# Optimization experiments

Measured on AMD Instinct MI355X. Metric: run time of the kernel, lower is better.

The kernel has to match this reference:

```python
import jax, jax.numpy as jnp
import numpy as np


def setup_inputs() -> dict:
    key = jax.random.key(0)
    k1, k2, k3, k4, k5 = jax.random.split(key, 5)
    N, E, C_in, C_out = 100000, 1600000, 64, 64
    x = jax.random.normal(k1, (N, C_in), dtype=jnp.float32)
    edge_index = jax.random.randint(k2, (2, E), 0, N, dtype=jnp.int64)
    edge_weight = jax.random.uniform(k3, (E,), dtype=jnp.float32)
    # Xavier-uniform Linear weights [out, in], zero biases (matches reset_parameters)
    bound = float(np.sqrt(6.0 / (C_in + C_out)))
    W_self = jax.random.uniform(k4, (C_out, C_in), dtype=jnp.float32, minval=-bound, maxval=bound)
    W_neigh = jax.random.uniform(k5, (C_out, C_in), dtype=jnp.float32, minval=-bound, maxval=bound)
    b_self = jnp.zeros((C_out,), dtype=jnp.float32)
    b_neigh = jnp.zeros((C_out,), dtype=jnp.float32)
    return {"x": x, "edge_index": edge_index, "edge_weight": edge_weight,
            "W_self": W_self, "b_self": b_self, "W_neigh": W_neigh, "b_neigh": b_neigh,
            "num_nodes": N}


def reference(x, edge_index, edge_weight, W_self, b_self, W_neigh, b_neigh, num_nodes):
    row, col = edge_index[0], edge_index[1]
    # gather source features, weight, scatter-add to destinations: [E, C] -> [N, C]
    message = x[col] * edge_weight[:, None]
    neigh_agg = jax.ops.segment_sum(message, row, num_segments=num_nodes)
    # two linear projections (torch Linear: y = x @ W.T + b)
    return x @ W_self.T + b_self + neigh_agg @ W_neigh.T + b_neigh
```

## Files before the change

kernel.cpp:

```cpp
#include <hip/hip_runtime.h>
#include <hip/hip_bf16.h>


#define C 64
#define BKT 128
#define MAXB 800
#define BINT 6144
#define CAP 2560

typedef __attribute__((ext_vector_type(8))) short bf16x8;
typedef __attribute__((ext_vector_type(4))) float f32x4;

__device__ inline unsigned short f2bf(float f) {
    union { __hip_bfloat16 h; unsigned short u; } c;
    c.h = __float2bfloat16(f);
    return c.u;
}

__device__ inline float bfhi(unsigned short u) {
    return __int_as_float(((int)u) << 16);
}

__global__ __launch_bounds__(256) void prep_kernel(
        const int* __restrict__ ei, int* __restrict__ bhist, int E, int NBK,
        const float* __restrict__ x, unsigned short* __restrict__ xb, int n4) {
    __shared__ int lh[MAXB];
    const int t = threadIdx.x;
    for (int i = t; i < NBK; i += 256) lh[i] = 0;
    __syncthreads();
    const int gtid = blockIdx.x * 256 + t;
    const int gs = gridDim.x * 256;
    for (int e = gtid; e < E; e += gs)
        atomicAdd(&lh[ei[e] >> 7], 1);
    __syncthreads();
    for (int i = t; i < NBK; i += 256)
        if (lh[i]) atomicAdd(&bhist[i], lh[i]);
    const float4* x4 = (const float4*)x;
    ushort4* xb4 = (ushort4*)xb;
    for (int i = gtid; i < n4; i += gs) {
        float4 v = x4[i];
        ushort4 o;
        o.x = f2bf(v.x); o.y = f2bf(v.y); o.z = f2bf(v.z); o.w = f2bf(v.w);
        xb4[i] = o;
    }
}

__global__ __launch_bounds__(1024) void scan_kernel(
        const int* __restrict__ bhist, int* __restrict__ boffs,
        int* __restrict__ bcur, int NBK) {
    __shared__ int s[1024];
    const int t = threadIdx.x;
    s[t] = (t < NBK) ? bhist[t] : 0;
    __syncthreads();
    for (int off = 1; off < 1024; off <<= 1) {
        int v = 0;
        if (t >= off) v = s[t - off];
        __syncthreads();
        if (t >= off) s[t] += v;
        __syncthreads();
    }
    if (t < NBK) {
        int e = (t > 0) ? s[t - 1] : 0;
        boffs[t] = e;
        bcur[t] = e;
        if (t == NBK - 1) boffs[NBK] = s[t];
    }
}

__global__ __launch_bounds__(256) void bin_kernel(
        const int* __restrict__ ei, const float* __restrict__ ew,
        int* __restrict__ bcur, const int* __restrict__ unused,
        int2* __restrict__ sorted, int E, int NBK) {
    __shared__ int2 stage[BINT];
    __shared__ int h[MAXB];
    __shared__ int ls[MAXB + 1];
    __shared__ int gb[MAXB];
    __shared__ int cur[MAXB];
    __shared__ int part[256];

    const int t = threadIdx.x;
    const int e0 = blockIdx.x * BINT;
    const int cnt = min(BINT, E - e0);

    for (int i = t; i < NBK; i += 256) h[i] = 0;
    __syncthreads();

#pragma unroll
    for (int k = 0; k < BINT / 256; ++k) {
        const int e = e0 + t + k * 256;
        if (e - e0 < cnt) atomicAdd(&h[ei[e] >> 7], 1);
    }
    __syncthreads();

    int vloc[4]; int s0 = 0;
#pragma unroll
    for (int k = 0; k < 4; ++k) {
        const int idx = t * 4 + k;
        vloc[k] = (idx < NBK) ? h[idx] : 0;
        s0 += vloc[k];
    }
    part[t] = s0;
    __syncthreads();
    for (int off = 1; off < 256; off <<= 1) {
        int v = 0;
        if (t >= off) v = part[t - off];
        __syncthreads();
        if (t >= off) part[t] += v;
        __syncthreads();
    }
    int run = (t > 0) ? part[t - 1] : 0;
#pragma unroll
    for (int k = 0; k < 4; ++k) {
        const int idx = t * 4 + k;
        if (idx < NBK) ls[idx] = run;
        run += vloc[k];
    }
    if (t == 255) ls[NBK] = part[255];
    __syncthreads();

    for (int i = t; i < NBK; i += 256) {
        const int hh = ls[i + 1] - ls[i];
        gb[i] = hh ? atomicAdd(&bcur[i], hh) : 0;
        cur[i] = ls[i];
    }
    __syncthreads();

#pragma unroll
    for (int k = 0; k < BINT / 256; ++k) {
        const int e = e0 + t + k * 256;
        if (e - e0 < cnt) {
            const int d = ei[e];
            const int s = ei[E + e];
            const float w = ew[e];
            const int b = d >> 7;
            const int dl = d & 127;
            const int p = atomicAdd(&cur[b], 1);
            stage[p] = make_int2((dl << 17) | s, __float_as_int(w));
        }
    }
    __syncthreads();

    for (int i = t; i < cnt; i += 256) {
        int lo = 0, hi = NBK - 1;
#pragma unroll
        for (int it = 0; it < 10; ++it) {
            const int mid = (lo + hi + 1) >> 1;
            if (ls[mid] <= i) lo = mid; else hi = mid - 1;
        }
        sorted[gb[lo] + (i - ls[lo])] = stage[i];
    }
}

__global__ __launch_bounds__(512) void agg_kernel(
        const ushort4* __restrict__ xb4,
        const int2* __restrict__ sorted,
        const int* __restrict__ boffs,
        float* __restrict__ agg, int N) {
    __shared__ int2 meta2[CAP];
    __shared__ int lcnt[BKT];
    __shared__ int lincl[BKT];
    __shared__ int lcur[BKT];

    const int t = threadIdx.x;
    const int b = blockIdx.x;
    const int node0 = b << 7;
    const int lane = t & 63;
    const int wv = t >> 6;
    const int q = lane >> 4;
    const int cq = lane & 15;

    const int beg = boffs[b];
    const int end = boffs[b + 1];

    int chunk = beg;
    do {
        const int cc = (end - chunk < CAP) ? (end - chunk) : CAP;

        for (int i = t; i < BKT; i += 512) lcnt[i] = 0;
        __syncthreads();

        for (int i = t; i < cc; i += 512)
            atomicAdd(&lcnt[sorted[chunk + i].x >> 17], 1);
        __syncthreads();

        if (t < BKT) lincl[t] = lcnt[t];
        __syncthreads();
        for (int off = 1; off < BKT; off <<= 1) {
            int v = 0;
            if (t < BKT && t >= off) v = lincl[t - off];
            __syncthreads();
            if (t < BKT && t >= off) lincl[t] += v;
            __syncthreads();
        }
        if (t < BKT) lcur[t] = lincl[t] - lcnt[t];
        __syncthreads();

        for (int i = t; i < cc; i += 512) {
            const int2 m = sorted[chunk + i];
            const int dl = m.x >> 17;
            const int p = atomicAdd(&lcur[dl], 1);
            meta2[p] = make_int2(m.x & 0x1FFFF, m.y);
        }
        __syncthreads();

        const bool first = (chunk == beg);
        for (int r = wv; r < BKT; r += 8) {
            const int s1 = lincl[r];
            const int s0 = s1 - lcnt[r];
            float a0 = 0.f, a1 = 0.f, a2 = 0.f, a3 = 0.f;
            int j = s0 + q;
            for (; j + 4 < s1; j += 8) {
                const int2 m0 = meta2[j];
                const int2 m1 = meta2[j + 4];
                const ushort4 u0 = xb4[(unsigned)m0.x * 16u + cq];
                const ushort4 u1 = xb4[(unsigned)m1.x * 16u + cq];
                const float w0 = __int_as_float(m0.y);
                const float w1 = __int_as_float(m1.y);
                a0 += w0 * bfhi(u0.x); a1 += w0 * bfhi(u0.y);
                a2 += w0 * bfhi(u0.z); a3 += w0 * bfhi(u0.w);
                a0 += w1 * bfhi(u1.x); a1 += w1 * bfhi(u1.y);
                a2 += w1 * bfhi(u1.z); a3 += w1 * bfhi(u1.w);
            }
            if (j < s1) {
                const int2 m0 = meta2[j];
                const ushort4 u0 = xb4[(unsigned)m0.x * 16u + cq];
                const float w0 = __int_as_float(m0.y);
                a0 += w0 * bfhi(u0.x); a1 += w0 * bfhi(u0.y);
                a2 += w0 * bfhi(u0.z); a3 += w0 * bfhi(u0.w);
            }
            a0 += __shfl_xor(a0, 16); a0 += __shfl_xor(a0, 32);
            a1 += __shfl_xor(a1, 16); a1 += __shfl_xor(a1, 32);
            a2 += __shfl_xor(a2, 16); a2 += __shfl_xor(a2, 32);
            a3 += __shfl_xor(a3, 16); a3 += __shfl_xor(a3, 32);
            const int node = node0 + r;
            if (q == 0 && node < N) {
                float4* dst = (float4*)(agg + (size_t)node * C + 4 * cq);
                if (first) {
                    *dst = make_float4(a0, a1, a2, a3);
                } else {
                    float4 o = *dst;
                    o.x += a0; o.y += a1; o.z += a2; o.w += a3;
                    *dst = o;
                }
            }
        }
        chunk += CAP;
        __syncthreads();
    } while (chunk < end);
}

__global__ __launch_bounds__(256) void scatter_kernel(
        const float* __restrict__ x, const int* __restrict__ ei,
        const float* __restrict__ ew, float* __restrict__ agg, int E) {
    const int lane = threadIdx.x & 63;
    const int wid = (blockIdx.x * blockDim.x + threadIdx.x) >> 6;
    const int nw = (gridDim.x * blockDim.x) >> 6;
    for (int base = wid * 64; base < E; base += nw * 64) {
        const int e = base + lane;
        int dst = 0, src = 0; float w = 0.f;
        if (e < E) { dst = ei[e]; src = ei[E + e]; w = ew[e]; }
        const int cnt = min(64, E - base);
        for (int j = 0; j < cnt; ++j) {
            const int d = __shfl(dst, j);
            const int s = __shfl(src, j);
            const float wj = __shfl(w, j);
            atomicAdd(&agg[d * C + lane], x[s * C + lane] * wj);
        }
    }
}

__device__ inline bf16x8 cvt8(const float* __restrict__ p) {
    f32x4 lo = *(const f32x4*)p;
    f32x4 hi = *(const f32x4*)(p + 4);
    union { bf16x8 v; __hip_bfloat16 e[8]; } u;
#pragma unroll
    for (int j = 0; j < 4; ++j) u.e[j] = __float2bfloat16(lo[j]);
#pragma unroll
    for (int j = 0; j < 4; ++j) u.e[4 + j] = __float2bfloat16(hi[j]);
    return u.v;
}

__global__ __launch_bounds__(256) void proj_kernel(
        const float* __restrict__ x, const float* __restrict__ agg,
        const float* __restrict__ Ws, const float* __restrict__ bs,
        const float* __restrict__ Wn, const float* __restrict__ bn,
        float* __restrict__ out, int N) {
    const int lane = threadIdx.x & 63;
    const int wid = (blockIdx.x * blockDim.x + threadIdx.x) >> 6;
    const int l15 = lane & 15;
    const int quad = lane >> 4;
    const int nTiles = N >> 4;
    if (wid >= nTiles) return;
    const int m0 = wid << 4;

    bf16x8 bsf[4][2], bnf[4][2];
#pragma unroll
    for (int tt = 0; tt < 4; ++tt) {
        const int o = tt * 16 + l15;
#pragma unroll
        for (int h = 0; h < 2; ++h) {
            bsf[tt][h] = cvt8(Ws + o * C + h * 32 + quad * 8);
            bnf[tt][h] = cvt8(Wn + o * C + h * 32 + quad * 8);
        }
    }

    const int m = m0 + l15;
    bf16x8 ax[2], ag[2];
#pragma unroll
    for (int h = 0; h < 2; ++h) {
        ax[h] = cvt8(x + m * C + h * 32 + quad * 8);
        ag[h] = cvt8(agg + m * C + h * 32 + quad * 8);
    }

#pragma unroll
    for (int tt = 0; tt < 4; ++tt) {
        f32x4 acc = {0.f, 0.f, 0.f, 0.f};
        acc = __builtin_amdgcn_mfma_f32_16x16x32_bf16(ax[0], bsf[tt][0], acc, 0, 0, 0);
        acc = __builtin_amdgcn_mfma_f32_16x16x32_bf16(ax[1], bsf[tt][1], acc, 0, 0, 0);
        acc = __builtin_amdgcn_mfma_f32_16x16x32_bf16(ag[0], bnf[tt][0], acc, 0, 0, 0);
        acc = __builtin_amdgcn_mfma_f32_16x16x32_bf16(ag[1], bnf[tt][1], acc, 0, 0, 0);
        const int o = tt * 16 + l15;
        const float bias = bs[o] + bn[o];
#pragma unroll
        for (int r = 0; r < 4; ++r)
            out[(m0 + quad * 4 + r) * C + o] = acc[r] + bias;
    }
}

extern "C" void kernel_launch(void* const* d_in, const int* in_sizes, int n_in,
                              void* d_out, int out_size, void* d_ws, size_t ws_size,
                              hipStream_t stream) {
    const float* x  = (const float*)d_in[0];
    const int*   ei = (const int*)d_in[1];
    const float* ew = (const float*)d_in[2];
    const float* Ws = (const float*)d_in[3];
    const float* bs = (const float*)d_in[4];
    const float* Wn = (const float*)d_in[5];
    const float* bn = (const float*)d_in[6];

    const int N = in_sizes[0] / C;
    const int E = in_sizes[2];
    const int NBK = (N + BKT - 1) / BKT;

    char* p = (char*)d_ws;
    float* agg = (float*)p;                 p += (size_t)N * C * sizeof(float);
    unsigned short* xb = (unsigned short*)p; p += (size_t)N * C * sizeof(short);
    int2* sorted = (int2*)p;                p += (size_t)E * sizeof(int2);
    int* bhist = (int*)p;                   p += (size_t)MAXB * sizeof(int);
    int* boffs = (int*)p;                   p += (size_t)(MAXB + 1) * sizeof(int);
    int* bcur = (int*)p;                    p += (size_t)MAXB * sizeof(int);
    const size_t needed = (size_t)(p - (char*)d_ws);

    const int nTiles = N / 16;
    const int projBlocks = (nTiles + 3) / 4;

    if (needed <= ws_size && N <= (1 << 17) && NBK <= MAXB) {
        const int n4 = N * C / 4;
        hipMemsetAsync(bhist, 0, (size_t)NBK * sizeof(int), stream);
        prep_kernel<<<1024, 256, 0, stream>>>(ei, bhist, E, NBK, x, xb, n4);
        scan_kernel<<<1, 1024, 0, stream>>>(bhist, boffs, bcur, NBK);
        bin_kernel<<<(E + BINT - 1) / BINT, 256, 0, stream>>>(ei, ew, bcur, bhist,
                                                              sorted, E, NBK);
        agg_kernel<<<NBK, 512, 0, stream>>>((const ushort4*)xb, sorted,
                                            boffs, agg, N);
    } else {
        hipMemsetAsync(agg, 0, (size_t)N * C * sizeof(float), stream);
        scatter_kernel<<<2048, 256, 0, stream>>>(x, ei, ew, agg, E);
    }

    proj_kernel<<<projBlocks, 256, 0, stream>>>(x, agg, Ws, bs, Wn, bn,
                                                (float*)d_out, N);
}
```

Measured before the change: 232.8 us.

## Restructure bin kernel: 1024 threads, wave-shuffle scan, stored bucket ids

The binning kernel now runs 1024 threads per block. Its bucket-offset scan uses wave shuffles in place of the multi-barrier shared-memory scan. Each staged edge also records its bucket id, so the scatter to global memory reads a precomputed offset instead of doing a 10-step binary search per edge. This cuts per-edge search cost and barrier count, in exchange for extra shared memory and a larger block, which may lower occupancy. The one-bucket-per-thread scan assumes NBK stays at or below 1024.

```diff
diff --git a/kernel.cpp b/kernel.cpp
--- a/kernel.cpp
+++ b/kernel.cpp
@@ -6,6 +6,7 @@
 #define BKT 128
 #define MAXB 800
 #define BINT 6144
+#define BTHR 1024
 #define CAP 2560
 
 typedef __attribute__((ext_vector_type(8))) short bf16x8;
@@ -67,68 +68,66 @@
     }
 }
 
-__global__ __launch_bounds__(256) void bin_kernel(
+__global__ __launch_bounds__(BTHR) void bin_kernel(
         const int* __restrict__ ei, const float* __restrict__ ew,
         int* __restrict__ bcur, const int* __restrict__ unused,
         int2* __restrict__ sorted, int E, int NBK) {
     __shared__ int2 stage[BINT];
+    __shared__ unsigned short stageb[BINT];
     __shared__ int h[MAXB];
-    __shared__ int ls[MAXB + 1];
-    __shared__ int gb[MAXB];
     __shared__ int cur[MAXB];
-    __shared__ int part[256];
+    __shared__ int adj[MAXB];
+    __shared__ int wsum[16];
 
     const int t = threadIdx.x;
+    const int lane = t & 63;
+    const int wv = t >> 6;
     const int e0 = blockIdx.x * BINT;
     const int cnt = min(BINT, E - e0);
 
-    for (int i = t; i < NBK; i += 256) h[i] = 0;
-    __syncthreads();
-
-#pragma unroll
-    for (int k = 0; k < BINT / 256; ++k) {
-        const int e = e0 + t + k * 256;
-        if (e - e0 < cnt) atomicAdd(&h[ei[e] >> 7], 1);
-    }
-    __syncthreads();
-
-    int vloc[4]; int s0 = 0;
-#pragma unroll
-    for (int k = 0; k < 4; ++k) {
-        const int idx = t * 4 + k;
-        vloc[k] = (idx < NBK) ? h[idx] : 0;
-        s0 += vloc[k];
-    }
-    part[t] = s0;
-    __syncthreads();
-    for (int off = 1; off < 256; off <<= 1) {
-        int v = 0;
-        if (t >= off) v = part[t - off];
-        __syncthreads();
-        if (t >= off) part[t] += v;
-        __syncthreads();
-    }
-    int run = (t > 0) ? part[t - 1] : 0;
-#pragma unroll
-    for (int k = 0; k < 4; ++k) {
-        const int idx = t * 4 + k;
-        if (idx < NBK) ls[idx] = run;
-        run += vloc[k];
-    }
-    if (t == 255) ls[NBK] = part[255];
-    __syncthreads();
-
-    for (int i = t; i < NBK; i += 256) {
-        const int hh = ls[i + 1] - ls[i];
-        gb[i] = hh ? atomicAdd(&bcur[i], hh) : 0;
-        cur[i] = ls[i];
-    }
-    __syncthreads();
-
-#pragma unroll
-    for (int k = 0; k < BINT / 256; ++k) {
-        const int e = e0 + t + k * 256;
-        if (e - e0 < cnt) {
+    for (int i = t; i < NBK; i += BTHR) h[i] = 0;
+    __syncthreads();
+
+#pragma unroll
+    for (int k = 0; k < BINT / BTHR; ++k) {
+        const int idx = t + k * BTHR;
+        if (idx < cnt) atomicAdd(&h[ei[e0 + idx] >> 7], 1);
+    }
+    __syncthreads();
+
+    const int val = (t < NBK) ? h[t] : 0;
+    int v = val;
+#pragma unroll
+    for (int off = 1; off < 64; off <<= 1) {
+        const int u = __shfl_up(v, off);
+        if (lane >= off) v += u;
+    }
+    if (lane == 63) wsum[wv] = v;
+    __syncthreads();
+    if (t < 64) {
+        int s = (lane < 16) ? wsum[lane] : 0;
+#pragma unroll
+        for (int off = 1; off < 16; off <<= 1) {
+            const int u = __shfl_up(s, off);
+            if (lane >= off) s += u;
+        }
+        if (lane < 16) wsum[lane] = s;
+    }
+    __syncthreads();
+    if (t < NBK) {
+        const int incl = v + ((wv > 0) ? wsum[wv - 1] : 0);
+        const int excl = incl - val;
+        cur[t] = excl;
+        const int g = val ? atomicAdd(&bcur[t], val) : 0;
+        adj[t] = g - excl;
+    }
+    __syncthreads();
+
+#pragma unroll
+    for (int k = 0; k < BINT / BTHR; ++k) {
+        const int idx = t + k * BTHR;
+        if (idx < cnt) {
+            const int e = e0 + idx;
             const int d = ei[e];
             const int s = ei[E + e];
             const float w = ew[e];
@@ -136,18 +135,14 @@
             const int dl = d & 127;
             const int p = atomicAdd(&cur[b], 1);
             stage[p] = make_int2((dl << 17) | s, __float_as_int(w));
-        }
-    }
-    __syncthreads();
-
-    for (int i = t; i < cnt; i += 256) {
-        int lo = 0, hi = NBK - 1;
-#pragma unroll
-        for (int it = 0; it < 10; ++it) {
-            const int mid = (lo + hi + 1) >> 1;
-            if (ls[mid] <= i) lo = mid; else hi = mid - 1;
-        }
-        sorted[gb[lo] + (i - ls[lo])] = stage[i];
+            stageb[p] = (unsigned short)b;
+        }
+    }
+    __syncthreads();
+
+    for (int i = t; i < cnt; i += BTHR) {
+        const int b = stageb[i];
+        sorted[adj[b] + i] = stage[i];
     }
 }
 
@@ -359,8 +354,8 @@
         hipMemsetAsync(bhist, 0, (size_t)NBK * sizeof(int), stream);
         prep_kernel<<<1024, 256, 0, stream>>>(ei, bhist, E, NBK, x, xb, n4);
         scan_kernel<<<1, 1024, 0, stream>>>(bhist, boffs, bcur, NBK);
-        bin_kernel<<<(E + BINT - 1) / BINT, 256, 0, stream>>>(ei, ew, bcur, bhist,
-                                                              sorted, E, NBK);
+        bin_kernel<<<(E + BINT - 1) / BINT, BTHR, 0, stream>>>(ei, ew, bcur, bhist,
+                                                               sorted, E, NBK);
         agg_kernel<<<NBK, 512, 0, stream>>>((const ushort4*)xb, sorted,
                                             boffs, agg, N);
     } else {
```

New measurement: 215.4 us. 1.08x faster.
